# Performance work log

Hardware: AMD Instinct MI355X
Metric: run time of the kernel (lower is better)

## Reference

```python
import jax, jax.numpy as jnp
import numpy as np

BATCH, SEQ, INPUT_DIM, HIDDEN = 128, 1024, 256, 512


def setup_inputs() -> dict:
    key = jax.random.key(0)
    k1, k2, k3 = jax.random.split(key, 3)
    scale_su = 1.0 / np.sqrt(HIDDEN + INPUT_DIM)
    scale_out = 1.0 / np.sqrt(HIDDEN)
    return {
        "x": jax.random.normal(k1, (BATCH, SEQ, INPUT_DIM), dtype=jnp.float32),
        "carry": jnp.zeros((BATCH, HIDDEN), dtype=jnp.float32),
        "W_su": jax.random.normal(k2, (HIDDEN + INPUT_DIM, HIDDEN), dtype=jnp.float32) * scale_su,
        "b_su": jnp.zeros((HIDDEN,), dtype=jnp.float32),
        "W_out": jax.random.normal(k3, (HIDDEN, 1), dtype=jnp.float32) * scale_out,
        "b_out": jnp.zeros((1,), dtype=jnp.float32),
    }


def reference(x, carry, W_su, b_su, W_out, b_out):
    # Split state_update kernel into z-part and x-part (equivalent to concat -> Dense).
    hidden = carry.shape[-1]
    W_z = W_su[:hidden]          # (H, H)
    W_x = W_su[hidden:]          # (D, H)

    # Precompute the input contribution for all timesteps in one big GEMM.
    xW = jnp.einsum('btd,dh->bth', x, W_x) + b_su  # (B, T, H)

    def step(z, xw_t):
        z_new = jnp.tanh(z @ W_z + xw_t)
        return z_new, None

    # scan over time (T leading): (T, B, H)
    z_last, _ = jax.lax.scan(step, carry, jnp.swapaxes(xW, 0, 1))
    out = z_last @ W_out + b_out  # (B, 1)
    return out, z_last
```

## Files before the change

kernel.cpp:

```cpp
#include <hip/hip_runtime.h>
#include <hip/hip_bf16.h>

typedef _Float16 f16;
typedef _Float16 f16x2 __attribute__((ext_vector_type(2)));
typedef _Float16 f16x4 __attribute__((ext_vector_type(4)));
typedef _Float16 f16x8 __attribute__((ext_vector_type(8)));
typedef float f32x4 __attribute__((ext_vector_type(4)));

#define BATCH 128
#define SEQ   1024
#define IND   256
#define HID   512

#if defined(__has_builtin)
#if __has_builtin(__builtin_amdgcn_fdot2)
#define HAVE_FDOT2 1
#endif
#endif

__device__ __forceinline__ float fdot2(f16x2 a, f16x2 b, float c) {
#ifdef HAVE_FDOT2
  return __builtin_amdgcn_fdot2(a, b, c, false);
#else
  return c + (float)a[0] * (float)b[0] + (float)a[1] * (float)b[1];
#endif
}

union v8u {
  f16x8 v;
  f16x2 h[4];
};

__device__ __forceinline__ float tanh_fast(float s) {
  float e = __expf(2.0f * s);
  return 1.0f - 2.0f / (e + 1.0f);
}

template <int CTRL>
__device__ __forceinline__ float fdpp(float x) {
  int i = __builtin_bit_cast(int, x);
  i = __builtin_amdgcn_mov_dpp(i, CTRL, 0xf, 0xf, false);
  return __builtin_bit_cast(float, i);
}

__global__ __launch_bounds__(256) void prep_kernel(const float* __restrict__ Wsu,
                                                   f16* __restrict__ WzT,
                                                   f16* __restrict__ WxT) {
  int g = blockIdx.x * 256 + threadIdx.x;
  int k = g >> 9;
  int h = g & 511;
  float v = Wsu[g];
  if (k < HID) WzT[h * HID + k] = (f16)v;
  else         WxT[h * IND + (k - HID)] = (f16)v;
}

__global__ __launch_bounds__(256, 2) void gemm1_kernel(const float* __restrict__ x,
                                                       const f16* __restrict__ WxT,
                                                       const float* __restrict__ bsu,
                                                       f16* __restrict__ xw) {
  __shared__ __align__(16) char smem[65536];
  f16x8* Bbuf0 = (f16x8*)smem;
  f16x8* Bbuf1 = (f16x8*)(smem + 32768);

  const int m0 = blockIdx.x * 64;
  const int tid = threadIdx.x;
  const int w = tid >> 6, l = tid & 63;
  const int r16 = l & 15;
  const int kg  = l >> 4;
  const int arow = m0 + w * 16 + r16;

  f32x4 acc[32];
#pragma unroll
  for (int nt = 0; nt < 32; ++nt) {
    float bv = bsu[nt * 16 + r16];
    acc[nt] = (f32x4){bv, bv, bv, bv};
  }

#pragma unroll
  for (int i = 0; i < 8; ++i) {
    int c = tid + 256 * i;
    int n = c >> 2;
    int g = c & 3;
    Bbuf0[g * 512 + n] = *(const f16x8*)&WxT[(size_t)n * IND + 0 + g * 8];
  }
  __syncthreads();

#pragma unroll
  for (int kb = 0; kb < 8; ++kb) {
    f16x8* Bc = (kb & 1) ? Bbuf1 : Bbuf0;
    f16x8* Bn = (kb & 1) ? Bbuf0 : Bbuf1;
    if (kb + 1 < 8) {
      const int k0n = (kb + 1) * 32;
#pragma unroll
      for (int i = 0; i < 8; ++i) {
        int c = tid + 256 * i;
        int n = c >> 2;
        int g = c & 3;
        Bn[g * 512 + n] = *(const f16x8*)&WxT[(size_t)n * IND + k0n + g * 8];
      }
    }
    const float4* ap = (const float4*)&x[(size_t)arow * IND + kb * 32 + kg * 8];
    float4 a0 = ap[0], a1 = ap[1];
    f16x8 afrag = {(f16)a0.x, (f16)a0.y, (f16)a0.z, (f16)a0.w,
                   (f16)a1.x, (f16)a1.y, (f16)a1.z, (f16)a1.w};
#pragma unroll
    for (int nt = 0; nt < 32; ++nt) {
      f16x8 bfrag = Bc[kg * 512 + nt * 16 + r16];
      acc[nt] = __builtin_amdgcn_mfma_f32_16x16x32_f16(afrag, bfrag, acc[nt], 0, 0, 0);
    }
    __syncthreads();
  }

  f16* Ot = (f16*)smem;
#pragma unroll
  for (int nt = 0; nt < 32; ++nt) {
#pragma unroll
    for (int r = 0; r < 4; ++r) {
      int row = w * 16 + kg * 4 + r;
      Ot[row * 512 + nt * 16 + r16] = (f16)acc[nt][r];
    }
  }
  __syncthreads();
#pragma unroll
  for (int i = 0; i < 16; ++i) {
    int c = tid + 256 * i;
    int row = c >> 6;
    int co = (c & 63) * 8;
    *(f16x8*)&xw[(size_t)(m0 + row) * HID + co] = *(const f16x8*)&Ot[row * 512 + co];
  }
}

__global__ __launch_bounds__(512, 2) void scan_kernel(
    const f16* __restrict__ WzT, const f16* __restrict__ xw,
    const float* __restrict__ carry, const float* __restrict__ Wout,
    const float* __restrict__ bout, float* __restrict__ outp) {
  __shared__ __align__(16) f16 zsh[2][512];
  __shared__ __align__(16) f16x8 wl6[8][512];
  __shared__ __align__(16) f16x8 wl7[8][512];
  __shared__ float red[512];

  const int b_ = blockIdx.x;
  const int tid = threadIdx.x;
  const int w = tid >> 6, l = tid & 63;
  const int kc = l & 7;
  const int hq = l >> 3;
  const int hbase = w * 64 + hq * 8;

  f16x2 wreg[6][32];
#pragma unroll
  for (int r = 0; r < 6; ++r) {
#pragma unroll
    for (int s = 0; s < 8; ++s) {
      v8u v;
      v.v = *(const f16x8*)&WzT[(hbase + r) * HID + kc * 64 + ((s ^ kc) & 7) * 8];
#pragma unroll
      for (int p = 0; p < 4; ++p) wreg[r][s * 4 + p] = v.h[p];
    }
  }
#pragma unroll
  for (int r = 0; r < 6; ++r) {
#pragma unroll
    for (int s = 0; s < 32; ++s) {
      unsigned u = __builtin_bit_cast(unsigned, wreg[r][s]);
      asm volatile("" : "+v"(u));
      wreg[r][s] = __builtin_bit_cast(f16x2, u);
    }
  }
#pragma unroll
  for (int s = 0; s < 8; ++s) {
    wl6[s][tid] = *(const f16x8*)&WzT[(hbase + 6) * HID + kc * 64 + ((s ^ kc) & 7) * 8];
    wl7[s][tid] = *(const f16x8*)&WzT[(hbase + 7) * HID + kc * 64 + ((s ^ kc) & 7) * 8];
  }

  zsh[0][tid] = (f16)carry[b_ * HID + tid];

  const int b0 = l & 1, b1 = (l >> 1) & 1, b2 = (l >> 2) & 1;
  const int myh = hbase + (b2 << 2) + (b0 << 1) + b1;

  float xw_cur = (float)xw[(size_t)b_ * SEQ * HID + myh];

  __syncthreads();

  float zlast = 0.f;
  for (int t = 0; t < SEQ; ++t) {
    const int p = t & 1;
    int tn = (t + 1 < SEQ) ? t + 1 : t;
    float xw_nxt = (float)xw[((size_t)b_ * SEQ + tn) * HID + myh];

    const f16* zb = &zsh[p][kc * 64];
    float a0 = 0.f, a1 = 0.f, a2 = 0.f, a3 = 0.f;
    float a4 = 0.f, a5 = 0.f, a6 = 0.f, a7 = 0.f;
#pragma unroll
    for (int s = 0; s < 8; ++s) {
      v8u zc, w6, w7;
      zc.v = *(const f16x8*)&zb[((s ^ kc) & 7) * 8];
      w6.v = wl6[s][tid];
      w7.v = wl7[s][tid];
#pragma unroll
      for (int q4 = 0; q4 < 4; ++q4) {
        f16x2 zp = zc.h[q4];
        int pi = s * 4 + q4;
        a0 = fdot2(zp, wreg[0][pi], a0);
        a1 = fdot2(zp, wreg[1][pi], a1);
        a2 = fdot2(zp, wreg[2][pi], a2);
        a3 = fdot2(zp, wreg[3][pi], a3);
        a4 = fdot2(zp, wreg[4][pi], a4);
        a5 = fdot2(zp, wreg[5][pi], a5);
        a6 = fdot2(zp, w6.h[q4], a6);
        a7 = fdot2(zp, w7.h[q4], a7);
      }
    }

    float n0_ = b2 ? a4 : a0, s0_ = b2 ? a0 : a4;
    float n1_ = b2 ? a5 : a1, s1_ = b2 ? a1 : a5;
    float n2_ = b2 ? a6 : a2, s2_ = b2 ? a2 : a6;
    float n3_ = b2 ? a7 : a3, s3_ = b2 ? a3 : a7;
    n0_ += fdpp<0x141>(s0_);
    n1_ += fdpp<0x141>(s1_);
    n2_ += fdpp<0x141>(s2_);
    n3_ += fdpp<0x141>(s3_);
    float m0_ = b0 ? n2_ : n0_, t0_ = b0 ? n0_ : n2_;
    float m1_ = b0 ? n3_ : n1_, t1_ = b0 ? n1_ : n3_;
    m0_ += fdpp<0xB1>(t0_);
    m1_ += fdpp<0xB1>(t1_);
    float f0_ = b1 ? m1_ : m0_, g0_ = b1 ? m0_ : m1_;
    float tot = f0_ + fdpp<0x4E>(g0_);

    float z = tanh_fast(tot + xw_cur);
    zlast = z;
    zsh[p ^ 1][myh] = (f16)z;
    __syncthreads();
    xw_cur = xw_nxt;
  }

  outp[BATCH + (size_t)b_ * HID + myh] = zlast;
  red[myh] = zlast * Wout[myh];
  __syncthreads();
  if (tid < 64) {
    float s2 = 0.f;
#pragma unroll
    for (int i = 0; i < 8; ++i) s2 += red[tid + 64 * i];
    red[tid] = s2;
  }
  __syncthreads();
  if (tid == 0) {
    float s3 = 0.f;
    for (int i = 0; i < 64; ++i) s3 += red[i];
    outp[b_] = s3 + bout[0];
  }
}

extern "C" void kernel_launch(void* const* d_in, const int* in_sizes, int n_in,
                              void* d_out, int out_size, void* d_ws, size_t ws_size,
                              hipStream_t stream) {
  const float* x     = (const float*)d_in[0];
  const float* carry = (const float*)d_in[1];
  const float* Wsu   = (const float*)d_in[2];
  const float* bsu   = (const float*)d_in[3];
  const float* Wout  = (const float*)d_in[4];
  const float* bout  = (const float*)d_in[5];
  float* outp = (float*)d_out;

  char* ws = (char*)d_ws;
  f16* WzT = (f16*)(ws);
  f16* WxT = (f16*)(ws + 512 * 1024);
  f16* xw  = (f16*)(ws + 768 * 1024);

  prep_kernel<<<dim3((768 * 512) / 256), 256, 0, stream>>>(Wsu, WzT, WxT);
  gemm1_kernel<<<dim3(BATCH * SEQ / 64), 256, 0, stream>>>(x, WxT, bsu, xw);
  scan_kernel<<<dim3(BATCH), 512, 0, stream>>>(WzT, xw, carry, Wout, bout, outp);
}
```

Baseline: 1.441 ms.

## Halve scan block to 256 threads with 16 hidden rows per lane group

```diff
diff --git a/kernel.cpp b/kernel.cpp
--- a/kernel.cpp
+++ b/kernel.cpp
@@ -130,13 +130,12 @@
   }
 }
 
-__global__ __launch_bounds__(512, 2) void scan_kernel(
+__global__ __launch_bounds__(256, 1) void scan_kernel(
     const f16* __restrict__ WzT, const f16* __restrict__ xw,
     const float* __restrict__ carry, const float* __restrict__ Wout,
     const float* __restrict__ bout, float* __restrict__ outp) {
   __shared__ __align__(16) f16 zsh[2][512];
-  __shared__ __align__(16) f16x8 wl6[8][512];
-  __shared__ __align__(16) f16x8 wl7[8][512];
+  __shared__ __align__(16) f16x8 wl[4][8][256];
   __shared__ float red[512];
 
   const int b_ = blockIdx.x;
@@ -144,21 +143,21 @@
   const int w = tid >> 6, l = tid & 63;
   const int kc = l & 7;
   const int hq = l >> 3;
-  const int hbase = w * 64 + hq * 8;
-
-  f16x2 wreg[6][32];
-#pragma unroll
-  for (int r = 0; r < 6; ++r) {
+  const int hb = w * 128 + hq * 16;
+
+  f16x2 wreg[12][32];
+#pragma unroll
+  for (int r = 0; r < 12; ++r) {
 #pragma unroll
     for (int s = 0; s < 8; ++s) {
       v8u v;
-      v.v = *(const f16x8*)&WzT[(hbase + r) * HID + kc * 64 + ((s ^ kc) & 7) * 8];
+      v.v = *(const f16x8*)&WzT[(size_t)(hb + r) * HID + kc * 64 + ((s ^ kc) & 7) * 8];
 #pragma unroll
       for (int p = 0; p < 4; ++p) wreg[r][s * 4 + p] = v.h[p];
     }
   }
 #pragma unroll
-  for (int r = 0; r < 6; ++r) {
+  for (int r = 0; r < 12; ++r) {
 #pragma unroll
     for (int s = 0; s < 32; ++s) {
       unsigned u = __builtin_bit_cast(unsigned, wreg[r][s]);
@@ -167,74 +166,94 @@
     }
   }
 #pragma unroll
-  for (int s = 0; s < 8; ++s) {
-    wl6[s][tid] = *(const f16x8*)&WzT[(hbase + 6) * HID + kc * 64 + ((s ^ kc) & 7) * 8];
-    wl7[s][tid] = *(const f16x8*)&WzT[(hbase + 7) * HID + kc * 64 + ((s ^ kc) & 7) * 8];
-  }
-
-  zsh[0][tid] = (f16)carry[b_ * HID + tid];
-
-  const int b0 = l & 1, b1 = (l >> 1) & 1, b2 = (l >> 2) & 1;
-  const int myh = hbase + (b2 << 2) + (b0 << 1) + b1;
-
-  float xw_cur = (float)xw[(size_t)b_ * SEQ * HID + myh];
-
-  __syncthreads();
-
-  float zlast = 0.f;
+  for (int j = 0; j < 4; ++j)
+#pragma unroll
+    for (int s = 0; s < 8; ++s)
+      wl[j][s][tid] = *(const f16x8*)&WzT[(size_t)(hb + 12 + j) * HID + kc * 64 + ((s ^ kc) & 7) * 8];
+
+  {
+    float2 c2 = *(const float2*)&carry[b_ * HID + 2 * tid];
+    *(f16x2*)&zsh[0][2 * tid] = (f16x2){(f16)c2.x, (f16)c2.y};
+  }
+
+  const int b0 = kc & 1, b1 = (kc >> 1) & 1, b2 = (kc >> 2) & 1;
+  const int myh = hb + (b2 << 3) + (b0 << 2) + (b1 << 1);
+
+  f16x2 xwv = *(const f16x2*)&xw[(size_t)b_ * SEQ * HID + myh];
+  float xc0 = (float)xwv[0], xc1 = (float)xwv[1];
+
+  __syncthreads();
+
+  float zl0 = 0.f, zl1 = 0.f;
   for (int t = 0; t < SEQ; ++t) {
     const int p = t & 1;
     int tn = (t + 1 < SEQ) ? t + 1 : t;
-    float xw_nxt = (float)xw[((size_t)b_ * SEQ + tn) * HID + myh];
+    f16x2 xn = *(const f16x2*)&xw[((size_t)b_ * SEQ + tn) * HID + myh];
 
     const f16* zb = &zsh[p][kc * 64];
-    float a0 = 0.f, a1 = 0.f, a2 = 0.f, a3 = 0.f;
-    float a4 = 0.f, a5 = 0.f, a6 = 0.f, a7 = 0.f;
+    float a[16];
+#pragma unroll
+    for (int r = 0; r < 16; ++r) a[r] = 0.f;
 #pragma unroll
     for (int s = 0; s < 8; ++s) {
-      v8u zc, w6, w7;
-      zc.v = *(const f16x8*)&zb[((s ^ kc) & 7) * 8];
-      w6.v = wl6[s][tid];
-      w7.v = wl7[s][tid];
-#pragma unroll
-      for (int q4 = 0; q4 < 4; ++q4) {
-        f16x2 zp = zc.h[q4];
-        int pi = s * 4 + q4;
-        a0 = fdot2(zp, wreg[0][pi], a0);
-        a1 = fdot2(zp, wreg[1][pi], a1);
-        a2 = fdot2(zp, wreg[2][pi], a2);
-        a3 = fdot2(zp, wreg[3][pi], a3);
-        a4 = fdot2(zp, wreg[4][pi], a4);
-        a5 = fdot2(zp, wreg[5][pi], a5);
-        a6 = fdot2(zp, w6.h[q4], a6);
-        a7 = fdot2(zp, w7.h[q4], a7);
+      v8u zc, w12, w13, w14, w15;
+      zc.v  = *(const f16x8*)&zb[((s ^ kc) & 7) * 8];
+      w12.v = wl[0][s][tid];
+      w13.v = wl[1][s][tid];
+      w14.v = wl[2][s][tid];
+      w15.v = wl[3][s][tid];
+#pragma unroll
+      for (int q = 0; q < 4; ++q) {
+        f16x2 zp = zc.h[q];
+        int pi = s * 4 + q;
+        a[0]  = fdot2(zp, wreg[0][pi],  a[0]);
+        a[1]  = fdot2(zp, wreg[1][pi],  a[1]);
+        a[2]  = fdot2(zp, wreg[2][pi],  a[2]);
+        a[3]  = fdot2(zp, wreg[3][pi],  a[3]);
+        a[4]  = fdot2(zp, wreg[4][pi],  a[4]);
+        a[5]  = fdot2(zp, wreg[5][pi],  a[5]);
+        a[6]  = fdot2(zp, wreg[6][pi],  a[6]);
+        a[7]  = fdot2(zp, wreg[7][pi],  a[7]);
+        a[8]  = fdot2(zp, wreg[8][pi],  a[8]);
+        a[9]  = fdot2(zp, wreg[9][pi],  a[9]);
+        a[10] = fdot2(zp, wreg[10][pi], a[10]);
+        a[11] = fdot2(zp, wreg[11][pi], a[11]);
+        a[12] = fdot2(zp, w12.h[q], a[12]);
+        a[13] = fdot2(zp, w13.h[q], a[13]);
+        a[14] = fdot2(zp, w14.h[q], a[14]);
+        a[15] = fdot2(zp, w15.h[q], a[15]);
       }
     }
 
-    float n0_ = b2 ? a4 : a0, s0_ = b2 ? a0 : a4;
-    float n1_ = b2 ? a5 : a1, s1_ = b2 ? a1 : a5;
-    float n2_ = b2 ? a6 : a2, s2_ = b2 ? a2 : a6;
-    float n3_ = b2 ? a7 : a3, s3_ = b2 ? a3 : a7;
-    n0_ += fdpp<0x141>(s0_);
-    n1_ += fdpp<0x141>(s1_);
-    n2_ += fdpp<0x141>(s2_);
-    n3_ += fdpp<0x141>(s3_);
-    float m0_ = b0 ? n2_ : n0_, t0_ = b0 ? n0_ : n2_;
-    float m1_ = b0 ? n3_ : n1_, t1_ = b0 ? n1_ : n3_;
-    m0_ += fdpp<0xB1>(t0_);
-    m1_ += fdpp<0xB1>(t1_);
-    float f0_ = b1 ? m1_ : m0_, g0_ = b1 ? m0_ : m1_;
-    float tot = f0_ + fdpp<0x4E>(g0_);
-
-    float z = tanh_fast(tot + xw_cur);
-    zlast = z;
-    zsh[p ^ 1][myh] = (f16)z;
+    float u[8];
+#pragma unroll
+    for (int j = 0; j < 8; ++j) {
+      float keep = b2 ? a[j + 8] : a[j];
+      float send = b2 ? a[j] : a[j + 8];
+      u[j] = keep + fdpp<0x141>(send);
+    }
+    float v[4];
+#pragma unroll
+    for (int j = 0; j < 4; ++j) {
+      float keep = b0 ? u[j + 4] : u[j];
+      float send = b0 ? u[j] : u[j + 4];
+      v[j] = keep + fdpp<0xB1>(send);
+    }
+    float t0 = (b1 ? v[2] : v[0]) + fdpp<0x4E>(b1 ? v[0] : v[2]);
+    float t1 = (b1 ? v[3] : v[1]) + fdpp<0x4E>(b1 ? v[1] : v[3]);
+
+    float z0 = tanh_fast(t0 + xc0);
+    float z1 = tanh_fast(t1 + xc1);
+    zl0 = z0; zl1 = z1;
+    *(f16x2*)&zsh[p ^ 1][myh] = (f16x2){(f16)z0, (f16)z1};
     __syncthreads();
-    xw_cur = xw_nxt;
-  }
-
-  outp[BATCH + (size_t)b_ * HID + myh] = zlast;
-  red[myh] = zlast * Wout[myh];
+    xc0 = (float)xn[0];
+    xc1 = (float)xn[1];
+  }
+
+  *(float2*)&outp[BATCH + (size_t)b_ * HID + myh] = (float2){zl0, zl1};
+  red[myh]     = zl0 * Wout[myh];
+  red[myh + 1] = zl1 * Wout[myh + 1];
   __syncthreads();
   if (tid < 64) {
     float s2 = 0.f;
@@ -268,5 +287,5 @@
 
   prep_kernel<<<dim3((768 * 512) / 256), 256, 0, stream>>>(Wsu, WzT, WxT);
   gemm1_kernel<<<dim3(BATCH * SEQ / 64), 256, 0, stream>>>(x, WxT, bsu, xw);
-  scan_kernel<<<dim3(BATCH), 512, 0, stream>>>(WzT, xw, carry, Wout, bout, outp);
-}
+  scan_kernel<<<dim3(BATCH), 256, 0, stream>>>(WzT, xw, carry, Wout, bout, outp);
+}
```

After: 2.410 ms. 67.2% more time.
